# Optimization experiments

Hardware: AMD Instinct MI355X
Metric: run time of the kernel (lower is better)

## Reference

```python
import jax, jax.numpy as jnp
import numpy as np

EMBED = 256
HEADS = 8
LEVELS = 1
POINTS = 4
HEAD_DIM = EMBED // HEADS  # 32
SPATIAL = [(200, 200)]     # static (H, W) per level
BS = 2
NQ = 40000
NV = sum(h * w for h, w in SPATIAL)


def setup_inputs() -> dict:
    key = jax.random.key(0)
    ks = jax.random.split(key, 12)
    s = 0.02
    inp = {
        "query": jax.random.normal(ks[0], (BS, NQ, EMBED), jnp.float32),
        "value": jax.random.normal(ks[1], (BS, NV, EMBED), jnp.float32),
        "reference_points": jax.random.uniform(ks[2], (BS, NQ, LEVELS, 2), jnp.float32),
        "spatial_shapes": jnp.array(SPATIAL, dtype=jnp.int32),
        "W_value": jax.random.normal(ks[3], (EMBED, EMBED), jnp.float32) * s,
        "b_value": jax.random.normal(ks[4], (EMBED,), jnp.float32) * s,
        "W_off": jax.random.normal(ks[5], (EMBED, HEADS * LEVELS * POINTS * 2), jnp.float32) * s,
        "b_off": jax.random.normal(ks[6], (HEADS * LEVELS * POINTS * 2,), jnp.float32) * s,
        "W_attn": jax.random.normal(ks[7], (EMBED, HEADS * LEVELS * POINTS), jnp.float32) * s,
        "b_attn": jax.random.normal(ks[8], (HEADS * LEVELS * POINTS,), jnp.float32) * s,
        "W_out": jax.random.normal(ks[9], (EMBED, EMBED), jnp.float32) * s,
        "b_out": jax.random.normal(ks[10], (EMBED,), jnp.float32) * s,
    }
    return inp


def _bilinear_sample(v_l, x, y, H, W):
    """grid_sample(bilinear, padding zeros, align_corners=False) on flat spatial.
    v_l: [bs, heads, H*W, d]; x, y: [bs, nq, heads, P] pixel coords.
    Returns [bs, nq, heads, P, d]."""
    bs = v_l.shape[0]
    nq = x.shape[1]
    x0 = jnp.floor(x)
    y0 = jnp.floor(y)
    out = jnp.zeros((bs, nq, HEADS, POINTS, HEAD_DIM), v_l.dtype)
    for dx in (0, 1):
        for dy in (0, 1):
            xi = x0 + dx
            yi = y0 + dy
            w = (1.0 - jnp.abs(x - xi)) * (1.0 - jnp.abs(y - yi))
            valid = (xi >= 0) & (xi <= W - 1) & (yi >= 0) & (yi <= H - 1)
            xi_c = jnp.clip(xi, 0, W - 1).astype(jnp.int32)
            yi_c = jnp.clip(yi, 0, H - 1).astype(jnp.int32)
            idx = yi_c * W + xi_c                               # [bs,nq,heads,P]
            idx = idx.transpose(0, 2, 1, 3).reshape(bs, HEADS, nq * POINTS)
            g = jnp.take_along_axis(v_l, idx[..., None], axis=2)  # [bs,heads,nq*P,d]
            g = g.reshape(bs, HEADS, nq, POINTS, HEAD_DIM).transpose(0, 2, 1, 3, 4)
            out = out + g * (w * valid.astype(w.dtype))[..., None]
    return out


def reference(query, value, reference_points, spatial_shapes,
              W_value, b_value, W_off, b_off, W_attn, b_attn, W_out, b_out):
    bs, nq, _ = query.shape
    # value projection
    v = (value @ W_value + b_value).reshape(bs, -1, HEADS, HEAD_DIM)
    v = v.transpose(0, 2, 1, 3)  # [bs, heads, nv, d]
    # sampling offsets and attention weights from query
    off = (query @ W_off + b_off).reshape(bs, nq, HEADS, LEVELS, POINTS, 2)
    aw = (query @ W_attn + b_attn).reshape(bs, nq, HEADS, LEVELS * POINTS)
    aw = jax.nn.softmax(aw, axis=-1).reshape(bs, nq, HEADS, LEVELS, POINTS)
    # sampling locations in [0,1] (reference_points last dim == 2 branch)
    normalizer = jnp.stack([spatial_shapes[:, 1], spatial_shapes[:, 0]], -1).astype(query.dtype)  # [L,2]=(W,H)
    loc = reference_points[:, :, None, :, None, :] + off / normalizer[None, None, None, :, None, :]
    out = jnp.zeros((bs, nq, HEADS, HEAD_DIM), query.dtype)
    start = 0
    for lvl, (H, W) in enumerate(SPATIAL):
        v_l = v[:, :, start:start + H * W]            # [bs,heads,HW,d]
        g = 2.0 * loc[:, :, :, lvl] - 1.0             # [bs,nq,heads,P,2] in [-1,1]
        px = ((g[..., 0] + 1.0) * W - 1.0) / 2.0      # align_corners=False
        py = ((g[..., 1] + 1.0) * H - 1.0) / 2.0
        sampled = _bilinear_sample(v_l, px, py, H, W)  # [bs,nq,heads,P,d]
        out = out + (sampled * aw[:, :, :, lvl, :, None]).sum(axis=3)
        start += H * W
    out = out.reshape(bs, nq, EMBED) @ W_out + b_out
    # dropout is identity in eval; identity residual = query (no query_pos)
    return out + query
```

## Files before the change

kernel.cpp:

```cpp
#include <hip/hip_runtime.h>


typedef float  f4  __attribute__((ext_vector_type(4)));
typedef float  fx4 __attribute__((ext_vector_type(4)));
typedef short  s8  __attribute__((ext_vector_type(8)));

#define M_TOT   80000
#define KDIM    256
#define NVPIX   40000
#define GH      200
#define GW      200

__device__ __forceinline__ short f2bf(float f) {
  union { float f; unsigned u; } v; v.f = f;
  unsigned r = v.u + 0x7fffu + ((v.u >> 16) & 1u);
  return (short)(r >> 16);
}
__device__ __forceinline__ float bf2f(unsigned short h) {
  union { unsigned u; float f; } v; v.u = ((unsigned)h) << 16; return v.f;
}

__global__ void prep_k(const float* __restrict__ Wv, const float* __restrict__ Wo,
                       const float* __restrict__ Woff, const float* __restrict__ Wattn,
                       const float* __restrict__ boff, const float* __restrict__ battn,
                       unsigned short* __restrict__ Wv_t, unsigned short* __restrict__ Wo_t,
                       unsigned short* __restrict__ Wp_t, float* __restrict__ bp)
{
  int i = blockIdx.x * 256 + threadIdx.x;
  if (i < 65536) {
    int n = i >> 8, k = i & 255;
    Wv_t[i] = (unsigned short)f2bf(Wv[k * 256 + n]);
  } else if (i < 131072) {
    int j = i - 65536; int n = j >> 8, k = j & 255;
    Wo_t[j] = (unsigned short)f2bf(Wo[k * 256 + n]);
  } else if (i < 163840) {
    int j = i - 131072; int n = j >> 8, k = j & 255;
    float val = (n < 64) ? Woff[k * 64 + n] : ((n < 96) ? Wattn[k * 32 + (n - 64)] : 0.f);
    Wp_t[j] = (unsigned short)f2bf(val);
  } else if (i < 163968) {
    int j = i - 163840;
    bp[j] = (j < 64) ? boff[j] : ((j < 96) ? battn[j - 64] : 0.f);
  }
}

template<int ABF, int CBF, int RES>
__global__ __launch_bounds__(256)
void gemm_k(const void* __restrict__ Ap, const unsigned short* __restrict__ Bt,
            const float* __restrict__ bias, const float* __restrict__ resid,
            void* __restrict__ Cp, int N)
{
  __shared__ short As[128 * 40];
  __shared__ short Bs[128 * 40];
  const int t  = threadIdx.x;
  const int m0 = blockIdx.x * 128;
  const int n0 = blockIdx.y * 128;
  const int sr = t >> 1;
  const int sk = (t & 1) * 16;
  const int lane = t & 63;
  const int w  = t >> 6;
  const int wm = (w >> 1) * 64;
  const int wn = (w & 1) * 64;
  const int fr = lane & 15;
  const int quad = lane >> 4;

  fx4 acc[4][4];
  #pragma unroll
  for (int i = 0; i < 4; i++)
    #pragma unroll
    for (int j = 0; j < 4; j++) { fx4 z = {0.f, 0.f, 0.f, 0.f}; acc[i][j] = z; }

  for (int k0 = 0; k0 < KDIM; k0 += 32) {
    __syncthreads();
    if (ABF) {
      const unsigned short* src = (const unsigned short*)Ap + (size_t)(m0 + sr) * KDIM + k0 + sk;
      s8 a0 = *(const s8*)(src);
      s8 a1 = *(const s8*)(src + 8);
      *(s8*)(&As[sr * 40 + sk])     = a0;
      *(s8*)(&As[sr * 40 + sk + 8]) = a1;
    } else {
      const float* src = (const float*)Ap + (size_t)(m0 + sr) * KDIM + k0 + sk;
      f4 f0 = *(const f4*)(src);
      f4 f1 = *(const f4*)(src + 4);
      f4 f2 = *(const f4*)(src + 8);
      f4 f3 = *(const f4*)(src + 12);
      s8 a0, a1;
      #pragma unroll
      for (int i = 0; i < 4; i++) {
        a0[i]     = f2bf(f0[i]);
        a0[i + 4] = f2bf(f1[i]);
        a1[i]     = f2bf(f2[i]);
        a1[i + 4] = f2bf(f3[i]);
      }
      *(s8*)(&As[sr * 40 + sk])     = a0;
      *(s8*)(&As[sr * 40 + sk + 8]) = a1;
    }
    {
      const unsigned short* src = Bt + (size_t)(n0 + sr) * KDIM + k0 + sk;
      s8 b0 = *(const s8*)(src);
      s8 b1 = *(const s8*)(src + 8);
      *(s8*)(&Bs[sr * 40 + sk])     = b0;
      *(s8*)(&Bs[sr * 40 + sk + 8]) = b1;
    }
    __syncthreads();

    s8 afr[4], bfr[4];
    #pragma unroll
    for (int i = 0; i < 4; i++) afr[i] = *(const s8*)(&As[(wm + i * 16 + fr) * 40 + quad * 8]);
    #pragma unroll
    for (int i = 0; i < 4; i++) bfr[i] = *(const s8*)(&Bs[(wn + i * 16 + fr) * 40 + quad * 8]);
    #pragma unroll
    for (int i = 0; i < 4; i++)
      #pragma unroll
      for (int j = 0; j < 4; j++)
        acc[i][j] = __builtin_amdgcn_mfma_f32_16x16x32_bf16(afr[i], bfr[j], acc[i][j], 0, 0, 0);
  }

  #pragma unroll
  for (int i = 0; i < 4; i++) {
    const int mbase = m0 + wm + i * 16 + quad * 4;
    #pragma unroll
    for (int j = 0; j < 4; j++) {
      const int n = n0 + wn + j * 16 + fr;
      const float bn = bias[n];
      #pragma unroll
      for (int r = 0; r < 4; r++) {
        const size_t m = (size_t)(mbase + r);
        float v = acc[i][j][r] + bn;
        if (RES) v += resid[m * (size_t)N + n];
        if (CBF) ((unsigned short*)Cp)[m * (size_t)N + n] = (unsigned short)f2bf(v);
        else     ((float*)Cp)[m * (size_t)N + n] = v;
      }
    }
  }
}

__global__ __launch_bounds__(256)
void sample_k(const unsigned short* __restrict__ v, const float* __restrict__ p,
              const float* __restrict__ ref, unsigned short* __restrict__ o)
{
  const int t  = threadIdx.x;
  const int q0 = blockIdx.x * 8;
  __shared__ float sp[8][128];
  __shared__ float sref[16];
  {
    const float* pb = p + (size_t)q0 * 128;
    #pragma unroll
    for (int j = 0; j < 4; j++) {
      int i = t + j * 256;
      sp[i >> 7][i & 127] = pb[i];
    }
    if (t < 16) sref[t] = ref[(size_t)q0 * 2 + t];
  }
  __syncthreads();

  const int qi = t >> 5;
  const int h  = (t >> 2) & 7;
  const int dg = t & 3;
  const int q  = q0 + qi;
  const int b  = (q >= 40000) ? 1 : 0;

  const float lg0 = sp[qi][64 + h * 4 + 0], lg1 = sp[qi][64 + h * 4 + 1];
  const float lg2 = sp[qi][64 + h * 4 + 2], lg3 = sp[qi][64 + h * 4 + 3];
  const float mx = fmaxf(fmaxf(lg0, lg1), fmaxf(lg2, lg3));
  const float e0 = __expf(lg0 - mx), e1 = __expf(lg1 - mx);
  const float e2 = __expf(lg2 - mx), e3 = __expf(lg3 - mx);
  const float inv = 1.f / (e0 + e1 + e2 + e3);
  const float aws[4] = {e0 * inv, e1 * inv, e2 * inv, e3 * inv};
  const float rx = sref[qi * 2], ry = sref[qi * 2 + 1];

  const unsigned short* vb = v + (size_t)b * NVPIX * 256;
  const int cbase = h * 32 + dg * 8;

  float acc[8];
  #pragma unroll
  for (int e = 0; e < 8; e++) acc[e] = 0.f;

  #pragma unroll
  for (int pt = 0; pt < 4; ++pt) {
    const float ox = sp[qi][h * 8 + pt * 2], oy = sp[qi][h * 8 + pt * 2 + 1];
    const float px = rx * 200.f + ox - 0.5f;
    const float py = ry * 200.f + oy - 0.5f;
    const float x0f = floorf(px), y0f = floorf(py);
    const int ix = (int)x0f, iy = (int)y0f;
    const float fx = px - x0f, fy = py - y0f;
    const float a = aws[pt];
    const float vx0 = (ix >= 0 && ix < GW) ? 1.f : 0.f;
    const float vx1 = (ix + 1 >= 0 && ix + 1 < GW) ? 1.f : 0.f;
    const float vy0 = (iy >= 0 && iy < GH) ? 1.f : 0.f;
    const float vy1 = (iy + 1 >= 0 && iy + 1 < GH) ? 1.f : 0.f;
    const float w00 = a * (1.f - fx) * (1.f - fy) * vx0 * vy0;
    const float w01 = a * fx * (1.f - fy) * vx1 * vy0;
    const float w10 = a * (1.f - fx) * fy * vx0 * vy1;
    const float w11 = a * fx * fy * vx1 * vy1;
    const int ix0c = min(max(ix, 0), GW - 1);
    const int ix1c = min(max(ix + 1, 0), GW - 1);
    const int iy0c = min(max(iy, 0), GH - 1);
    const int iy1c = min(max(iy + 1, 0), GH - 1);
    const int r0 = iy0c * (GW * 256) + cbase;
    const int r1 = iy1c * (GW * 256) + cbase;
    s8 g00 = *(const s8*)(vb + r0 + ix0c * 256);
    s8 g01 = *(const s8*)(vb + r0 + ix1c * 256);
    s8 g10 = *(const s8*)(vb + r1 + ix0c * 256);
    s8 g11 = *(const s8*)(vb + r1 + ix1c * 256);
    #pragma unroll
    for (int e = 0; e < 8; e++) {
      acc[e] += w00 * bf2f((unsigned short)g00[e]) + w01 * bf2f((unsigned short)g01[e])
              + w10 * bf2f((unsigned short)g10[e]) + w11 * bf2f((unsigned short)g11[e]);
    }
  }

  s8 res;
  #pragma unroll
  for (int e = 0; e < 8; e++) res[e] = f2bf(acc[e]);
  *(s8*)(o + (size_t)q * 256 + cbase) = res;
}

extern "C" void kernel_launch(void* const* d_in, const int* in_sizes, int n_in,
                              void* d_out, int out_size, void* d_ws, size_t ws_size,
                              hipStream_t stream)
{
  const float* query = (const float*)d_in[0];
  const float* value = (const float*)d_in[1];
  const float* refp  = (const float*)d_in[2];
  const float* Wv    = (const float*)d_in[4];
  const float* bv    = (const float*)d_in[5];
  const float* Woff  = (const float*)d_in[6];
  const float* boff  = (const float*)d_in[7];
  const float* Wattn = (const float*)d_in[8];
  const float* battn = (const float*)d_in[9];
  const float* Wo    = (const float*)d_in[10];
  const float* bo    = (const float*)d_in[11];

  char* ws = (char*)d_ws;
  unsigned short* ws_v = (unsigned short*)ws;
  float*          ws_p = (float*)(ws + 40960000);
  unsigned short* ws_o = (unsigned short*)(ws + 81920000);
  unsigned short* Wv_t = (unsigned short*)(ws + 122880000);
  unsigned short* Wo_t = Wv_t + 65536;
  unsigned short* Wp_t = Wo_t + 65536;
  float*          bp   = (float*)(Wp_t + 32768);

  hipLaunchKernelGGL(prep_k, dim3(641), dim3(256), 0, stream,
                     Wv, Wo, Woff, Wattn, boff, battn, Wv_t, Wo_t, Wp_t, bp);
  hipLaunchKernelGGL((gemm_k<0, 1, 0>), dim3(625, 2), dim3(256), 0, stream,
                     (const void*)value, Wv_t, bv, (const float*)nullptr, (void*)ws_v, 256);
  hipLaunchKernelGGL((gemm_k<0, 0, 0>), dim3(625, 1), dim3(256), 0, stream,
                     (const void*)query, Wp_t, bp, (const float*)nullptr, (void*)ws_p, 128);
  hipLaunchKernelGGL(sample_k, dim3(10000), dim3(256), 0, stream,
                     ws_v, ws_p, refp, ws_o);
  hipLaunchKernelGGL((gemm_k<1, 0, 1>), dim3(625, 2), dim3(256), 0, stream,
                     (const void*)ws_o, Wo_t, bo, query, (void*)d_out, 256);
}
```

Before: 408.0 us.

## Prefetch next K-tile into registers and widen GEMM K-step to 64

Restructures the bf16 MFMA GEMM main loop so global loads for the next 64-wide K slice are issued into registers before the current slice's MFMAs run. This overlaps global memory latency with compute. The K step doubles from 32 to 64, with LDS row padding of 68, which halves the number of barrier pairs. Loads are also made more coalesced per row. In exchange, register pressure rises, especially in the fp32-A path that holds eight float4 values, and LDS use grows.

```diff
diff --git a/kernel.cpp b/kernel.cpp
--- a/kernel.cpp
+++ b/kernel.cpp
@@ -4,12 +4,13 @@
 typedef float  f4  __attribute__((ext_vector_type(4)));
 typedef float  fx4 __attribute__((ext_vector_type(4)));
 typedef short  s8  __attribute__((ext_vector_type(8)));
-
-#define M_TOT   80000
+typedef short  s4  __attribute__((ext_vector_type(4)));
+
 #define KDIM    256
 #define NVPIX   40000
 #define GH      200
 #define GW      200
+#define LDP     68
 
 __device__ __forceinline__ short f2bf(float f) {
   union { float f; unsigned u; } v; v.f = f;
@@ -49,13 +50,11 @@
             const float* __restrict__ bias, const float* __restrict__ resid,
             void* __restrict__ Cp, int N)
 {
-  __shared__ short As[128 * 40];
-  __shared__ short Bs[128 * 40];
+  __shared__ short As[128 * LDP];
+  __shared__ short Bs[128 * LDP];
   const int t  = threadIdx.x;
   const int m0 = blockIdx.x * 128;
   const int n0 = blockIdx.y * 128;
-  const int sr = t >> 1;
-  const int sk = (t & 1) * 16;
   const int lane = t & 63;
   const int w  = t >> 6;
   const int wm = (w >> 1) * 64;
@@ -69,50 +68,87 @@
     #pragma unroll
     for (int j = 0; j < 4; j++) { fx4 z = {0.f, 0.f, 0.f, 0.f}; acc[i][j] = z; }
 
-  for (int k0 = 0; k0 < KDIM; k0 += 32) {
+  f4 pa[8];
+  s8 pa8[4];
+  s8 pb[4];
+
+  auto loadA = [&](int k0) {
+    if (ABF) {
+      const unsigned short* base = (const unsigned short*)Ap + (size_t)m0 * KDIM + k0;
+      #pragma unroll
+      for (int j = 0; j < 4; j++) {
+        int id = t + j * 256;
+        int row = id >> 3, kp = (id & 7) * 8;
+        pa8[j] = *(const s8*)(base + (size_t)row * KDIM + kp);
+      }
+    } else {
+      const float* base = (const float*)Ap + (size_t)m0 * KDIM + k0;
+      #pragma unroll
+      for (int j = 0; j < 8; j++) {
+        int id = t + j * 256;
+        int row = id >> 4, kp = (id & 15) * 4;
+        pa[j] = *(const f4*)(base + (size_t)row * KDIM + kp);
+      }
+    }
+  };
+  auto loadB = [&](int k0) {
+    const unsigned short* base = Bt + (size_t)n0 * KDIM + k0;
+    #pragma unroll
+    for (int j = 0; j < 4; j++) {
+      int id = t + j * 256;
+      int row = id >> 3, kp = (id & 7) * 8;
+      pb[j] = *(const s8*)(base + (size_t)row * KDIM + kp);
+    }
+  };
+  auto storeAB = [&]() {
+    if (ABF) {
+      #pragma unroll
+      for (int j = 0; j < 4; j++) {
+        int id = t + j * 256;
+        int row = id >> 3, kp = (id & 7) * 8;
+        *(s8*)(&As[row * LDP + kp]) = pa8[j];
+      }
+    } else {
+      #pragma unroll
+      for (int j = 0; j < 8; j++) {
+        int id = t + j * 256;
+        int row = id >> 4, kp = (id & 15) * 4;
+        s4 c;
+        #pragma unroll
+        for (int e = 0; e < 4; e++) c[e] = f2bf(pa[j][e]);
+        *(s4*)(&As[row * LDP + kp]) = c;
+      }
+    }
+    #pragma unroll
+    for (int j = 0; j < 4; j++) {
+      int id = t + j * 256;
+      int row = id >> 3, kp = (id & 7) * 8;
+      *(s8*)(&Bs[row * LDP + kp]) = pb[j];
+    }
+  };
+
+  loadA(0); loadB(0);
+  #pragma unroll
+  for (int it = 0; it < 4; ++it) {
     __syncthreads();
-    if (ABF) {
-      const unsigned short* src = (const unsigned short*)Ap + (size_t)(m0 + sr) * KDIM + k0 + sk;
-      s8 a0 = *(const s8*)(src);
-      s8 a1 = *(const s8*)(src + 8);
-      *(s8*)(&As[sr * 40 + sk])     = a0;
-      *(s8*)(&As[sr * 40 + sk + 8]) = a1;
-    } else {
-      const float* src = (const float*)Ap + (size_t)(m0 + sr) * KDIM + k0 + sk;
-      f4 f0 = *(const f4*)(src);
-      f4 f1 = *(const f4*)(src + 4);
-      f4 f2 = *(const f4*)(src + 8);
-      f4 f3 = *(const f4*)(src + 12);
-      s8 a0, a1;
-      #pragma unroll
-      for (int i = 0; i < 4; i++) {
-        a0[i]     = f2bf(f0[i]);
-        a0[i + 4] = f2bf(f1[i]);
-        a1[i]     = f2bf(f2[i]);
-        a1[i + 4] = f2bf(f3[i]);
-      }
-      *(s8*)(&As[sr * 40 + sk])     = a0;
-      *(s8*)(&As[sr * 40 + sk + 8]) = a1;
-    }
-    {
-      const unsigned short* src = Bt + (size_t)(n0 + sr) * KDIM + k0 + sk;
-      s8 b0 = *(const s8*)(src);
-      s8 b1 = *(const s8*)(src + 8);
-      *(s8*)(&Bs[sr * 40 + sk])     = b0;
-      *(s8*)(&Bs[sr * 40 + sk + 8]) = b1;
-    }
+    storeAB();
     __syncthreads();
-
-    s8 afr[4], bfr[4];
-    #pragma unroll
-    for (int i = 0; i < 4; i++) afr[i] = *(const s8*)(&As[(wm + i * 16 + fr) * 40 + quad * 8]);
-    #pragma unroll
-    for (int i = 0; i < 4; i++) bfr[i] = *(const s8*)(&Bs[(wn + i * 16 + fr) * 40 + quad * 8]);
-    #pragma unroll
-    for (int i = 0; i < 4; i++)
-      #pragma unroll
-      for (int j = 0; j < 4; j++)
-        acc[i][j] = __builtin_amdgcn_mfma_f32_16x16x32_bf16(afr[i], bfr[j], acc[i][j], 0, 0, 0);
+    if (it < 3) { loadA((it + 1) * 64); loadB((it + 1) * 64); }
+    #pragma unroll
+    for (int kk = 0; kk < 2; kk++) {
+      s8 afr[4], bfr[4];
+      #pragma unroll
+      for (int i = 0; i < 4; i++)
+        afr[i] = *(const s8*)(&As[(wm + i * 16 + fr) * LDP + kk * 32 + quad * 8]);
+      #pragma unroll
+      for (int i = 0; i < 4; i++)
+        bfr[i] = *(const s8*)(&Bs[(wn + i * 16 + fr) * LDP + kk * 32 + quad * 8]);
+      #pragma unroll
+      for (int i = 0; i < 4; i++)
+        #pragma unroll
+        for (int j = 0; j < 4; j++)
+          acc[i][j] = __builtin_amdgcn_mfma_f32_16x16x32_bf16(afr[i], bfr[j], acc[i][j], 0, 0, 0);
+    }
   }
 
   #pragma unroll
```

Measured after the change: 353.5 us. 13.4% less time.
